# Optimization experiments

Hardware: AMD Instinct MI355X
Metric: run time of the kernel (lower is better)

The kernel has to match this reference:

```python
import jax, jax.numpy as jnp
import numpy as np

NUM_CLASSES = 80
STRIDES = (8, 16, 32)


def _decode(p, stride):
    # p: [B, 5+C, H, W] raw head -> [B, HW, 5+C] decoded (xy in px, wh=exp*stride)
    B, C, H, W = p.shape
    ys, xs = jnp.meshgrid(jnp.arange(H), jnp.arange(W), indexing='ij')
    grid = jnp.stack([xs, ys], -1).reshape(H * W, 2).astype(p.dtype)
    out = p.reshape(B, C, H * W).transpose(0, 2, 1)
    xy = (out[..., :2] + grid) * stride
    wh = jnp.exp(out[..., 2:4]) * stride
    out = jnp.concatenate([xy, wh, out[..., 4:]], -1)
    es = jnp.full((H * W,), float(stride), p.dtype)
    return out, grid[:, 0], grid[:, 1], es


def _pairwise_iou(gt, pr):
    # gt [G,4] cxcywh, pr [A,4] -> [G,A]
    gt_tl = gt[:, None, :2] - gt[:, None, 2:] * 0.5
    gt_br = gt[:, None, :2] + gt[:, None, 2:] * 0.5
    pr_tl = pr[None, :, :2] - pr[None, :, 2:] * 0.5
    pr_br = pr[None, :, :2] + pr[None, :, 2:] * 0.5
    tl = jnp.maximum(gt_tl, pr_tl)
    br = jnp.minimum(gt_br, pr_br)
    en = jnp.all(tl < br, -1).astype(gt.dtype)
    inter = jnp.prod(br - tl, -1) * en
    a_gt = jnp.prod(gt[:, 2:], -1)[:, None]
    a_pr = jnp.prod(pr[:, 2:], -1)[None, :]
    return inter / (a_gt + a_pr - inter + 1e-16)


def _assign(gt_boxes, gt_cls, bbox, clsp, objp, xg, yg, es):
    # SimOTA assignment for one image (all fixed-shape; non-candidate anchors
    # are masked out via huge cost instead of boolean gather).
    G = gt_boxes.shape[0]
    xc = (xg + 0.5) * es  # [A] anchor centers
    yc = (yg + 0.5) * es
    gl = gt_boxes[:, 0:1] - 0.5 * gt_boxes[:, 2:3]
    gr = gt_boxes[:, 0:1] + 0.5 * gt_boxes[:, 2:3]
    gt_ = gt_boxes[:, 1:2] - 0.5 * gt_boxes[:, 3:4]
    gb = gt_boxes[:, 1:2] + 0.5 * gt_boxes[:, 3:4]
    in_box = (xc[None] > gl) & (xc[None] < gr) & (yc[None] > gt_) & (yc[None] < gb)  # [G,A]
    r = 2.5 * es[None]
    in_ctr = ((xc[None] > gt_boxes[:, 0:1] - r) & (xc[None] < gt_boxes[:, 0:1] + r)
              & (yc[None] > gt_boxes[:, 1:2] - r) & (yc[None] < gt_boxes[:, 1:2] + r))
    fg_cand = jnp.any(in_box, 0) | jnp.any(in_ctr, 0)  # [A]
    in_both = in_box & in_ctr  # [G,A]

    ious = _pairwise_iou(gt_boxes, bbox)  # [G,A]
    ious_m = jnp.where(fg_cand[None, :], ious, 0.0)
    iou_cost = -jnp.log(ious_m + 1e-8)

    # pairwise cls BCE cost: bce(sqrt(sigmoid(cls)*sigmoid(obj)), onehot(gt)).sum(-1)
    p = jnp.sqrt(jax.nn.sigmoid(clsp) * jax.nn.sigmoid(objp[:, None]))  # [A,C]
    lp = jnp.maximum(jnp.log(p), -100.0)
    l1p = jnp.maximum(jnp.log1p(-p), -100.0)
    t = jax.nn.one_hot(gt_cls, NUM_CLASSES, dtype=p.dtype)  # [G,C]
    cls_cost = -(jnp.einsum('ac,gc->ga', lp - l1p, t) + jnp.sum(l1p, -1)[None, :])

    cost = (cls_cost + 3.0 * iou_cost
            + 1e5 * (~in_both).astype(p.dtype)
            + 1e9 * (~fg_cand)[None, :].astype(p.dtype))

    # dynamic-k: k_g = clamp(sum(top10 ious), min=1)
    topk_ious, _ = jax.lax.top_k(ious_m, 10)
    dyn_k = jnp.clip(topk_ious.sum(-1).astype(jnp.int32), 1, None)  # [G]
    rank = jnp.argsort(jnp.argsort(cost, axis=1), axis=1)  # rank of each anchor per gt
    matching = (rank < dyn_k[:, None]) & fg_cand[None, :]  # [G,A]
    # resolve anchors matched to multiple gts: keep min-cost gt
    multi = matching.sum(0) > 1
    best = jnp.argmin(cost, 0)
    matching = jnp.where(multi[None, :], jnp.arange(G)[:, None] == best[None, :], matching)

    fg = jnp.any(matching, 0)  # [A]
    matched_gt = jnp.argmax(matching, 0)  # [A]
    pred_iou = jnp.sum(matching * ious, 0)  # [A]
    matched_cls = gt_cls[matched_gt]
    return fg, matched_gt, pred_iou, matched_cls


def _giou_loss(b, g):
    tl = jnp.maximum(b[..., :2] - b[..., 2:] * 0.5, g[..., :2] - g[..., 2:] * 0.5)
    br = jnp.minimum(b[..., :2] + b[..., 2:] * 0.5, g[..., :2] + g[..., 2:] * 0.5)
    area_b = jnp.prod(b[..., 2:], -1)
    area_g = jnp.prod(g[..., 2:], -1)
    en = jnp.all(tl < br, -1).astype(b.dtype)
    inter = jnp.prod(br - tl, -1) * en
    union = area_b + area_g - inter
    iou = inter / (union + 1e-16)
    ctl = jnp.minimum(b[..., :2] - b[..., 2:] * 0.5, g[..., :2] - g[..., 2:] * 0.5)
    cbr = jnp.maximum(b[..., :2] + b[..., 2:] * 0.5, g[..., :2] + g[..., 2:] * 0.5)
    area_c = jnp.maximum(jnp.prod(cbr - ctl, -1), 1e-16)
    giou = iou - (area_c - union) / area_c
    return 1.0 - jnp.clip(giou, -1.0, 1.0)


def _bce_logits(x, t):
    return jnp.maximum(x, 0.0) - x * t + jnp.log1p(jnp.exp(-jnp.abs(x)))


def _forward(p8, p16, p32, labels):
    outs, xo, yo, eo = [], [], [], []
    for p, s in zip((p8, p16, p32), STRIDES):
        o, x, y, e = _decode(p, s)
        outs.append(o); xo.append(x); yo.append(y); eo.append(e)
    outputs = jnp.concatenate(outs, 1)  # [B, A, 5+C]
    xg = jnp.concatenate(xo); yg = jnp.concatenate(yo); es = jnp.concatenate(eo)

    bbox = outputs[..., :4]
    obj = outputs[..., 4]
    cls = outputs[..., 5:]
    gt_boxes = labels[..., :4]
    gt_cls = labels[..., 4].astype(jnp.int32)

    # assignment runs under no_grad in torch
    det = jax.lax.stop_gradient(outputs)
    fg, matched_gt, pred_iou, matched_cls = jax.vmap(
        lambda gb, gc, o: _assign(gb, gc, o[..., :4], o[..., 5:], o[..., 4], xg, yg, es)
    )(gt_boxes, gt_cls, det)

    fgf = fg.astype(outputs.dtype)  # [B,A]
    reg_t = jnp.take_along_axis(gt_boxes, matched_gt[..., None], axis=1)  # [B,A,4]
    cls_t = (jax.nn.one_hot(matched_cls, NUM_CLASSES, dtype=outputs.dtype)
             * pred_iou[..., None] * fgf[..., None])

    loss_iou = jnp.sum(_giou_loss(bbox, reg_t) * fgf)
    loss_obj = jnp.sum(_bce_logits(obj, fgf))
    loss_cls = jnp.sum(_bce_logits(cls, cls_t) * fgf[..., None])
    num_fg = jnp.maximum(jnp.sum(fgf), 1.0)
    return (5.0 * loss_iou + loss_obj + loss_cls) / num_fg


def setup_inputs() -> dict:
    key = jax.random.key(0)
    k1, k2, k3, k4, k5, k6 = jax.random.split(key, 6)
    B, NGT = 32, 20
    p8 = jax.random.normal(k1, (B, 5 + NUM_CLASSES, 80, 80), dtype=jnp.float32)
    p16 = jax.random.normal(k2, (B, 5 + NUM_CLASSES, 40, 40), dtype=jnp.float32)
    p32 = jax.random.normal(k3, (B, 5 + NUM_CLASSES, 20, 20), dtype=jnp.float32)
    cxy = jax.random.uniform(k4, (B, NGT, 2), dtype=jnp.float32, minval=32.0, maxval=608.0)
    wh = jax.random.uniform(k5, (B, NGT, 2), dtype=jnp.float32, minval=16.0, maxval=128.0)
    cls = jax.random.randint(k6, (B, NGT, 1), 0, NUM_CLASSES).astype(jnp.float32)
    labels = jnp.concatenate([cxy, wh, cls], -1)
    return {"p8": p8, "p16": p16, "p32": p32, "labels": labels}


def reference(p8, p16, p32, labels):
    return _forward(p8, p16, p32, labels)
```

## Files before the change

kernel.cpp:

```cpp
#include <hip/hip_runtime.h>
#include <cstdint>
#include <cstddef>

#define NA 8400
#define NAP 8448
#define NB 32
#define NG 20
#define NCL 80
#define NBLK 33

__device__ __forceinline__ float frcp(float x) { return __builtin_amdgcn_rcpf(x); }
__device__ __forceinline__ float bce0(float x) {
  return fmaxf(x, 0.0f) + __logf(1.0f + __expf(-fabsf(x)));
}

__device__ __forceinline__ void anchor_info(int a, const float* p8, const float* p16,
                                            const float* p32, int b, const float*& base,
                                            int& hw, int& HW, int& xg, int& yg, float& fs) {
  if (a < 6400)      { hw = a;        HW = 6400; xg = hw % 80; yg = hw / 80; fs = 8.f;
                       base = p8  + (size_t)b * 85 * 6400; }
  else if (a < 8000) { hw = a - 6400; HW = 1600; xg = hw % 40; yg = hw / 40; fs = 16.f;
                       base = p16 + (size_t)b * 85 * 1600; }
  else               { hw = a - 8000; HW = 400;  xg = hw % 20; yg = hw / 20; fs = 32.f;
                       base = p32 + (size_t)b * 85 * 400; }
}

__device__ __forceinline__ float iou_raw(float gx, float gy, float gw, float gh, float4 p) {
  float gtlx = gx - gw * 0.5f, gtly = gy - gh * 0.5f;
  float gbrx = gx + gw * 0.5f, gbry = gy + gh * 0.5f;
  float ptlx = p.x - p.z * 0.5f, ptly = p.y - p.w * 0.5f;
  float pbrx = p.x + p.z * 0.5f, pbry = p.y + p.w * 0.5f;
  float tlx = fmaxf(gtlx, ptlx), tly = fmaxf(gtly, ptly);
  float brx = fminf(gbrx, pbrx), bry = fminf(gbry, pbry);
  float inter = ((tlx < brx) && (tly < bry)) ? (brx - tlx) * (bry - tly) : 0.0f;
  float ag = gw * gh, ap = p.z * p.w;
  return inter * frcp(ag + ap - inter + 1e-16f);
}

__device__ __forceinline__ float cost_from_x(float x, float lso, float slr,
                                             unsigned int am, int g,
                                             float gx, float gy, float gw, float gh,
                                             float4 pb, float& iou_out) {
  float u = __logf(1.0f + __expf(-fabsf(x)));
  float lsx = fminf(x, 0.0f) - u;
  float lpr = 0.5f * (lsx + lso);
  float p   = __expf(lpr);
  float l1p = fmaxf(__logf(1.0f - p), -100.0f);
  float wv  = fmaxf(lpr, -100.0f) - l1p;
  float iou = iou_raw(gx, gy, gw, gh, pb);
  iou_out = iou;
  float cst = -(wv + slr) - 3.0f * __logf(iou + 1e-8f);
  if (!((am >> g) & 1u)) cst += 100000.0f;
  return cst;
}

__device__ __forceinline__ float giou_loss(float4 bb, float gx, float gy, float gw, float gh) {
  float btlx = bb.x - bb.z * 0.5f, btly = bb.y - bb.w * 0.5f;
  float bbrx = bb.x + bb.z * 0.5f, bbry = bb.y + bb.w * 0.5f;
  float gtlx = gx - gw * 0.5f, gtly = gy - gh * 0.5f;
  float gbrx = gx + gw * 0.5f, gbry = gy + gh * 0.5f;
  float tlx = fmaxf(btlx, gtlx), tly = fmaxf(btly, gtly);
  float brx = fminf(bbrx, gbrx), bry = fminf(bbry, gbry);
  float area_b = bb.z * bb.w, area_g = gw * gh;
  float inter = ((tlx < brx) && (tly < bry)) ? (brx - tlx) * (bry - tly) : 0.0f;
  float uni = area_b + area_g - inter;
  float iou = inter / (uni + 1e-16f);
  float ctlx = fminf(btlx, gtlx), ctly = fminf(btly, gtly);
  float cbrx = fmaxf(bbrx, gbrx), cbry = fmaxf(bbry, gbry);
  float area_c = fmaxf((cbrx - ctlx) * (cbry - ctly), 1e-16f);
  float giou = iou - (area_c - uni) / area_c;
  giou = fminf(fmaxf(giou, -1.0f), 1.0f);
  return 1.0f - giou;
}

__global__ __launch_bounds__(256) void kA(const float* __restrict__ p8,
                                          const float* __restrict__ p16,
                                          const float* __restrict__ p32,
                                          const float* __restrict__ labels,
                                          int* __restrict__ n_fg_cnt,
                                          float4* __restrict__ meta_c,
                                          float4* __restrict__ bbox_c,
                                          float* __restrict__ sb_c,
                                          float* __restrict__ x_tbl,
                                          unsigned int* __restrict__ match_c,
                                          float* __restrict__ blk_obj) {
  __shared__ float s_gt[NG * 4];
  __shared__ unsigned int s_c2g[NCL];
  __shared__ unsigned int s_wcnt[4];
  __shared__ float s_part[4];
  __shared__ unsigned int s_base;

  int blk = blockIdx.x, b = blockIdx.y, tid = threadIdx.x, lane = tid & 63, wid = tid >> 6;
  size_t bo = (size_t)b * NAP;

  if (tid < NCL) s_c2g[tid] = 0u;
  __syncthreads();
  if (tid < NG) {
    s_gt[tid * 4 + 0] = labels[((size_t)b * NG + tid) * 5 + 0];
    s_gt[tid * 4 + 1] = labels[((size_t)b * NG + tid) * 5 + 1];
    s_gt[tid * 4 + 2] = labels[((size_t)b * NG + tid) * 5 + 2];
    s_gt[tid * 4 + 3] = labels[((size_t)b * NG + tid) * 5 + 3];
    int c = (int)labels[((size_t)b * NG + tid) * 5 + 4];
    atomicOr(&s_c2g[c], 1u << tid);
  }
  __syncthreads();

  int a = blk * 256 + tid;
  match_c[bo + a] = 0u;
  bool fg = false;
  unsigned int msk = 0u;
  float bce_obj = 0.0f, obj = 0.0f;
  const float* base = nullptr; int hw = 0, HW = 0, xg = 0, yg = 0; float fs = 8.f;
  if (a < NA) {
    anchor_info(a, p8, p16, p32, b, base, hw, HW, xg, yg, fs);
    obj = base[4 * HW + hw];
    bce_obj = bce0(obj);
    float xc = ((float)xg + 0.5f) * fs;
    float yc = ((float)yg + 0.5f) * fs;
    float r = 2.5f * fs;
#pragma unroll
    for (int g = 0; g < NG; ++g) {
      float gx = s_gt[g * 4 + 0], gy = s_gt[g * 4 + 1];
      float gw = s_gt[g * 4 + 2], gh = s_gt[g * 4 + 3];
      bool inb = (xc > gx - 0.5f * gw) && (xc < gx + 0.5f * gw) &&
                 (yc > gy - 0.5f * gh) && (yc < gy + 0.5f * gh);
      bool inc = (xc > gx - r) && (xc < gx + r) && (yc > gy - r) && (yc < gy + r);
      fg = fg || inb || inc;
      if (inb && inc) msk |= (1u << g);
    }
  }

  unsigned long long bm = __ballot(fg);
#pragma unroll
  for (int off = 32; off; off >>= 1) bce_obj += __shfl_down(bce_obj, off, 64);
  if (lane == 0) { s_wcnt[wid] = (unsigned int)__popcll(bm); s_part[wid] = bce_obj; }
  __syncthreads();
  if (tid == 0) {
    unsigned int cnt = s_wcnt[0] + s_wcnt[1] + s_wcnt[2] + s_wcnt[3];
    s_base = cnt ? (unsigned int)atomicAdd(&n_fg_cnt[b], (int)cnt) : 0u;
    blk_obj[b * NBLK + blk] = s_part[0] + s_part[1] + s_part[2] + s_part[3];
  }
  __syncthreads();

  int ci = -1;
  if (fg) {
    unsigned int li = 0;
    for (int w = 0; w < wid; ++w) li += s_wcnt[w];
    li += (unsigned int)__popcll(bm & ((1ull << lane) - 1ull));
    ci = (int)(s_base + li);
  }

  float lso = 0.0f;
  if (a < NA) {
    float uo = __logf(1.0f + __expf(-fabsf(obj)));
    lso = fminf(obj, 0.0f) - uo;
  }

  float sb = 0.0f, sl = 0.0f;
  if (a < NA) {
    const float* cb = base + (size_t)5 * HW + hw;
#pragma unroll 8
    for (int c = 0; c < NCL; ++c) {
      float x = cb[(size_t)c * HW];
      float u = __logf(1.0f + __expf(-fabsf(x)));
      sb += fmaxf(x, 0.0f) + u;
      float lsx = fminf(x, 0.0f) - u;
      float lpr = 0.5f * (lsx + lso);
      float p   = __expf(lpr);
      sl += fmaxf(__logf(1.0f - p), -100.0f);
      unsigned int m = s_c2g[c];
      if (fg && m) {
        do {
          int g = __ffs(m) - 1; m &= m - 1u;
          x_tbl[((size_t)b * NG + g) * NAP + ci] = x;
        } while (m);
      }
    }
  }

  if (!fg) return;

  float v0 = base[hw];
  float v1 = base[HW + hw];
  float v2 = base[2 * HW + hw];
  float v3 = base[3 * HW + hw];
  float4 bb4 = make_float4((v0 + (float)xg) * fs, (v1 + (float)yg) * fs,
                           __expf(v2) * fs, __expf(v3) * fs);
  bbox_c[bo + ci] = bb4;
  sb_c[bo + ci] = sb;
  meta_c[bo + ci] = make_float4(lso, sl, __uint_as_float(msk), obj);
}

__global__ __launch_bounds__(256) void kBG(const float* __restrict__ labels,
                                           const int* __restrict__ n_fg,
                                           const float4* __restrict__ meta_c,
                                           const float4* __restrict__ bbox_c,
                                           const float* __restrict__ sb_c,
                                           const float* __restrict__ x_tbl,
                                           unsigned int* __restrict__ match_c,
                                           const float* __restrict__ blk_obj,
                                           float* __restrict__ accum,
                                           int* __restrict__ done_g,
                                           int* __restrict__ done_img,
                                           float* __restrict__ out) {
  __shared__ float s_gt[NG * 5];
  __shared__ float s_wt[4 * 10];
  __shared__ float s_wc[4 * 10];
  __shared__ int   s_wi[4 * 10];
  __shared__ float s_red[16];
  __shared__ int   s_flag;

  int g = blockIdx.x, b = blockIdx.y, tid = threadIdx.x;
  int lane = tid & 63, wid = tid >> 6;
  int n = n_fg[b];
  size_t bo = (size_t)b * NAP;
  const float* __restrict__ xrow = x_tbl + ((size_t)b * NG + g) * NAP;

  if (tid < NG * 5) s_gt[tid] = labels[(size_t)b * NG * 5 + tid];
  __syncthreads();

  float ggx = s_gt[g * 5], ggy = s_gt[g * 5 + 1];
  float ggw = s_gt[g * 5 + 2], ggh = s_gt[g * 5 + 3];

  float t10[10];
  float c10v[10];
  int   c10i[10];
#pragma unroll
  for (int j = 0; j < 10; ++j) { t10[j] = 0.0f; c10v[j] = 3.4e38f; c10i[j] = 0x7fffffff; }

  for (int ci = tid; ci < n; ci += 256) {
    float4 me = meta_c[bo + ci];
    float4 pb = bbox_c[bo + ci];
    float x = xrow[ci];
    unsigned int am = __float_as_uint(me.z);
    float iou;
    float cst = cost_from_x(x, me.x, me.y, am, g, ggx, ggy, ggw, ggh, pb, iou);
    if (iou > t10[9]) {
      t10[9] = iou;
#pragma unroll
      for (int q = 9; q > 0; --q) {
        if (t10[q] > t10[q - 1]) { float t = t10[q]; t10[q] = t10[q - 1]; t10[q - 1] = t; }
        else break;
      }
    }
    if (cst < c10v[9] || (cst == c10v[9] && ci < c10i[9])) {
      c10v[9] = cst; c10i[9] = ci;
#pragma unroll
      for (int q = 9; q > 0; --q) {
        if (c10v[q] < c10v[q - 1] ||
            (c10v[q] == c10v[q - 1] && c10i[q] < c10i[q - 1])) {
          float tv = c10v[q]; c10v[q] = c10v[q - 1]; c10v[q - 1] = tv;
          int   ti = c10i[q]; c10i[q] = c10i[q - 1]; c10i[q - 1] = ti;
        } else break;
      }
    }
  }

  for (int r = 0; r < 10; ++r) {
    float v = t10[0];
    float bv = v;
    float cv = c10v[0]; int cix = c10i[0];
    float cbv = cv;     int cbi = cix;
#pragma unroll
    for (int off = 32; off; off >>= 1) {
      bv = fmaxf(bv, __shfl_down(bv, off, 64));
      float ov = __shfl_down(cbv, off, 64);
      int   oi = __shfl_down(cbi, off, 64);
      if (ov < cbv || (ov == cbv && oi < cbi)) { cbv = ov; cbi = oi; }
    }
    bv  = __shfl(bv, 0, 64);
    cbv = __shfl(cbv, 0, 64);
    cbi = __shfl(cbi, 0, 64);
    unsigned long long won = __ballot(v == bv);
    if (lane == __ffsll(won) - 1) {
#pragma unroll
      for (int q = 0; q < 9; ++q) t10[q] = t10[q + 1];
      t10[9] = -1.0f;
    }
    if (cv == cbv && cix == cbi) {
#pragma unroll
      for (int q = 0; q < 9; ++q) { c10v[q] = c10v[q + 1]; c10i[q] = c10i[q + 1]; }
      c10v[9] = 3.4e38f; c10i[9] = 0x7fffffff;
    }
    if (lane == 0) {
      s_wt[wid * 10 + r] = bv;
      s_wc[wid * 10 + r] = cbv;
      s_wi[wid * 10 + r] = cbi;
    }
  }
  __syncthreads();

  if (tid == 0) {
    int p0 = 0, p1 = 0, p2 = 0, p3 = 0;
    float s = 0.0f;
    for (int r = 0; r < 10; ++r) {
      float v0 = (p0 < 10) ? s_wt[p0]      : -2.0f;
      float v1 = (p1 < 10) ? s_wt[10 + p1] : -2.0f;
      float v2 = (p2 < 10) ? s_wt[20 + p2] : -2.0f;
      float v3 = (p3 < 10) ? s_wt[30 + p3] : -2.0f;
      float m = fmaxf(fmaxf(v0, v1), fmaxf(v2, v3));
      s += m;
      if (m == v0) ++p0; else if (m == v1) ++p1; else if (m == v2) ++p2; else ++p3;
    }
    int k = (int)s;
    if (k < 1) k = 1;
    int q[4] = {0, 0, 0, 0};
    for (int it = 0; it < k; ++it) {
      float bv = 3.3e38f; int bi = 0x7fffffff; int sel = -1;
#pragma unroll
      for (int w = 0; w < 4; ++w) {
        if (q[w] < 10) {
          float v = s_wc[w * 10 + q[w]];
          int   i = s_wi[w * 10 + q[w]];
          if (v < bv || (v == bv && i < bi)) { bv = v; bi = i; sel = w; }
        }
      }
      if (sel < 0 || bv >= 1e37f) break;
      atomicOr(&match_c[bo + bi], 1u << g);
      ++q[sel];
    }
    __threadfence();
    s_flag = (atomicAdd(&done_g[b], 1) == NG - 1) ? 1 : 0;
  }
  __syncthreads();
  if (!s_flag) return;

  float li = 0.0f, oe = 0.0f, lc = 0.0f, nf = 0.0f;
  for (int ci = tid; ci < n; ci += 256) {
    unsigned int m = atomicOr(&match_c[bo + ci], 0u);
    if (m == 0u) continue;
    float4 me = meta_c[bo + ci];
    float4 pb = bbox_c[bo + ci];
    unsigned int am = __float_as_uint(me.z);
    int mg;
    if (m & (m - 1)) {
      float bestc = 3.4e38f; mg = 0;
      for (int gq = 0; gq < NG; ++gq) {
        float xq = x_tbl[((size_t)b * NG + gq) * NAP + ci];
        float iouq;
        float cq = cost_from_x(xq, me.x, me.y, am, gq, s_gt[gq * 5], s_gt[gq * 5 + 1],
                               s_gt[gq * 5 + 2], s_gt[gq * 5 + 3], pb, iouq);
        if (cq < bestc) { bestc = cq; mg = gq; }
      }
    } else {
      mg = __ffs(m) - 1;
    }
    float gx = s_gt[mg * 5], gy = s_gt[mg * 5 + 1];
    float gw = s_gt[mg * 5 + 2], gh = s_gt[mg * 5 + 3];
    float piou = iou_raw(gx, gy, gw, gh, pb);
    li += giou_loss(pb, gx, gy, gw, gh);
    float xcls = x_tbl[((size_t)b * NG + mg) * NAP + ci];
    lc += sb_c[bo + ci] - xcls * piou;
    oe += me.w;
    nf += 1.0f;
  }

  float vals[4] = {li, oe, lc, nf};
#pragma unroll
  for (int q2 = 0; q2 < 4; ++q2) {
#pragma unroll
    for (int off = 32; off; off >>= 1) vals[q2] += __shfl_down(vals[q2], off, 64);
  }
  if (lane == 0) {
    s_red[wid * 4 + 0] = vals[0];
    s_red[wid * 4 + 1] = vals[1];
    s_red[wid * 4 + 2] = vals[2];
    s_red[wid * 4 + 3] = vals[3];
  }
  __syncthreads();
  if (tid < 4) {
    const int slot[4] = {0, 2, 3, 4};
    float s = s_red[tid] + s_red[4 + tid] + s_red[8 + tid] + s_red[12 + tid];
    atomicAdd(&accum[slot[tid]], s);
  }

  if (tid == 0) {
    __threadfence();
    s_flag = (atomicAdd(done_img, 1) == NB - 1) ? 1 : 0;
  }
  __syncthreads();
  if (!s_flag) return;

  float s = 0.0f;
  for (int i = tid; i < NB * NBLK; i += 256) s += blk_obj[i];
#pragma unroll
  for (int off = 32; off; off >>= 1) s += __shfl_down(s, off, 64);
  if ((tid & 63) == 0) s_red[tid >> 6] = s;
  __syncthreads();
  if (tid == 0) {
    float obj_base = s_red[0] + s_red[1] + s_red[2] + s_red[3];
    float loss_iou = atomicAdd(&accum[0], 0.0f);
    float oex      = atomicAdd(&accum[2], 0.0f);
    float loss_cls = atomicAdd(&accum[3], 0.0f);
    float num_fg   = atomicAdd(&accum[4], 0.0f);
    float loss_obj = obj_base - oex;
    out[0] = (5.0f * loss_iou + loss_obj + loss_cls) / fmaxf(num_fg, 1.0f);
  }
}

extern "C" void kernel_launch(void* const* d_in, const int* in_sizes, int n_in,
                              void* d_out, int out_size, void* d_ws, size_t ws_size,
                              hipStream_t stream) {
  const float* p8     = (const float*)d_in[0];
  const float* p16    = (const float*)d_in[1];
  const float* p32    = (const float*)d_in[2];
  const float* labels = (const float*)d_in[3];
  float* out = (float*)d_out;

  const size_t BAP = (size_t)NB * NAP;
  char* w = (char*)d_ws;
  float4*       bbox_c   = (float4*)w;
  float4*       meta_c   = (float4*)(w + BAP * 16);
  float*        x_tbl    = (float*)(w + BAP * 32);
  char*         w2       = (char*)x_tbl + (size_t)NB * NG * NAP * 4;
  float*        sb_c     = (float*)(w2);
  unsigned int* match_c  = (unsigned int*)(w2 + BAP * 4);
  char*         w3       = w2 + BAP * 8;
  int*          n_fg     = (int*)w3;
  float*        accum    = (float*)(w3 + 128);
  int*          done_g   = (int*)(w3 + 256);
  int*          done_img = (int*)(w3 + 384);
  float*        blk_obj  = (float*)(w3 + 512);

  hipMemsetAsync(w3, 0, 512, stream);

  kA <<<dim3(NBLK, NB), dim3(256), 0, stream>>>(p8, p16, p32, labels, n_fg, meta_c,
                                                bbox_c, sb_c, x_tbl, match_c, blk_obj);
  kBG<<<dim3(NG, NB), dim3(256), 0, stream>>>(labels, n_fg, meta_c, bbox_c, sb_c, x_tbl,
                                              match_c, blk_obj, accum, done_g,
                                              done_img, out);
}
```

Baseline: 200.0 us.

## Split class-loop across warps with float4 vectorized loads and LDS reduction

Instead of each thread looping over all 80 class logits for its own anchor, each of the four warps now handles 20 classes for four consecutive anchors per lane, using float4 loads. Partial BCE sums are reduced through shared memory, and each thread's candidate index and obj log-sigmoid are shared through LDS. This shortens the per-thread dependent loop and widens memory transactions. In exchange it adds shared memory, extra barriers, and alignment assumptions on the float4 loads (HW values are multiples of 4, so the loads stay aligned).

```diff
diff --git a/kernel.cpp b/kernel.cpp
--- a/kernel.cpp
+++ b/kernel.cpp
@@ -86,6 +86,10 @@
                                           float* __restrict__ blk_obj) {
   __shared__ float s_gt[NG * 4];
   __shared__ unsigned int s_c2g[NCL];
+  __shared__ float s_lso[256];
+  __shared__ int   s_ci[256];
+  __shared__ float s_sb[4][256];
+  __shared__ float s_sl[4][256];
   __shared__ unsigned int s_wcnt[4];
   __shared__ float s_part[4];
   __shared__ unsigned int s_base;
@@ -142,53 +146,81 @@
   }
   __syncthreads();
 
+  float lso = 0.0f;
+  if (a < NA) {
+    float uo = __logf(1.0f + __expf(-fabsf(obj)));
+    lso = fminf(obj, 0.0f) - uo;
+  }
+  s_lso[tid] = lso;
+
   int ci = -1;
   if (fg) {
     unsigned int li = 0;
     for (int w = 0; w < wid; ++w) li += s_wcnt[w];
     li += (unsigned int)__popcll(bm & ((1ull << lane) - 1ull));
     ci = (int)(s_base + li);
-  }
-
-  float lso = 0.0f;
-  if (a < NA) {
-    float uo = __logf(1.0f + __expf(-fabsf(obj)));
-    lso = fminf(obj, 0.0f) - uo;
-  }
-
-  float sb = 0.0f, sl = 0.0f;
-  if (a < NA) {
-    const float* cb = base + (size_t)5 * HW + hw;
-#pragma unroll 8
-    for (int c = 0; c < NCL; ++c) {
-      float x = cb[(size_t)c * HW];
-      float u = __logf(1.0f + __expf(-fabsf(x)));
-      sb += fmaxf(x, 0.0f) + u;
-      float lsx = fminf(x, 0.0f) - u;
-      float lpr = 0.5f * (lsx + lso);
-      float p   = __expf(lpr);
-      sl += fmaxf(__logf(1.0f - p), -100.0f);
+    float v0 = base[hw];
+    float v1 = base[HW + hw];
+    float v2 = base[2 * HW + hw];
+    float v3 = base[3 * HW + hw];
+    bbox_c[bo + ci] = make_float4((v0 + (float)xg) * fs, (v1 + (float)yg) * fs,
+                                  __expf(v2) * fs, __expf(v3) * fs);
+  }
+  s_ci[tid] = ci;
+  __syncthreads();
+
+  int a0 = blk * 256 + (lane << 2);
+  bool valid = a0 < NA;
+  const float* vbase = nullptr; int vhw = 0, vHW = 0, dxg, dyg; float dfs;
+  if (valid) anchor_info(a0, p8, p16, p32, b, vbase, vhw, vHW, dxg, dyg, dfs);
+  float l4[4], sb4[4] = {0.f, 0.f, 0.f, 0.f}, sl4[4] = {0.f, 0.f, 0.f, 0.f};
+  int   ci4[4];
+#pragma unroll
+  for (int j = 0; j < 4; ++j) {
+    l4[j]  = s_lso[(lane << 2) + j];
+    ci4[j] = s_ci[(lane << 2) + j];
+  }
+
+  if (valid) {
+    const float* cb = vbase + (size_t)5 * vHW + vhw;
+#pragma unroll 4
+    for (int cc = 0; cc < 20; ++cc) {
+      int c = wid * 20 + cc;
+      float4 x4 = *reinterpret_cast<const float4*>(cb + (size_t)c * vHW);
+      float xa[4] = {x4.x, x4.y, x4.z, x4.w};
+#pragma unroll
+      for (int j = 0; j < 4; ++j) {
+        float x = xa[j];
+        float u = __logf(1.0f + __expf(-fabsf(x)));
+        sb4[j] += fmaxf(x, 0.0f) + u;
+        float lsx = fminf(x, 0.0f) - u;
+        float lpr = 0.5f * (lsx + l4[j]);
+        float p   = __expf(lpr);
+        sl4[j] += fmaxf(__logf(1.0f - p), -100.0f);
+      }
       unsigned int m = s_c2g[c];
-      if (fg && m) {
-        do {
-          int g = __ffs(m) - 1; m &= m - 1u;
-          x_tbl[((size_t)b * NG + g) * NAP + ci] = x;
-        } while (m);
-      }
-    }
-  }
-
-  if (!fg) return;
-
-  float v0 = base[hw];
-  float v1 = base[HW + hw];
-  float v2 = base[2 * HW + hw];
-  float v3 = base[3 * HW + hw];
-  float4 bb4 = make_float4((v0 + (float)xg) * fs, (v1 + (float)yg) * fs,
-                           __expf(v2) * fs, __expf(v3) * fs);
-  bbox_c[bo + ci] = bb4;
-  sb_c[bo + ci] = sb;
-  meta_c[bo + ci] = make_float4(lso, sl, __uint_as_float(msk), obj);
+      while (m) {
+        int g = __ffs(m) - 1; m &= m - 1u;
+        size_t rowo = ((size_t)b * NG + g) * NAP;
+#pragma unroll
+        for (int j = 0; j < 4; ++j)
+          if (ci4[j] >= 0) x_tbl[rowo + ci4[j]] = xa[j];
+      }
+    }
+  }
+#pragma unroll
+  for (int j = 0; j < 4; ++j) {
+    s_sb[wid][(lane << 2) + j] = sb4[j];
+    s_sl[wid][(lane << 2) + j] = sl4[j];
+  }
+  __syncthreads();
+
+  if (ci >= 0) {
+    float sb = ((s_sb[0][tid] + s_sb[1][tid]) + s_sb[2][tid]) + s_sb[3][tid];
+    float sl = ((s_sl[0][tid] + s_sl[1][tid]) + s_sl[2][tid]) + s_sl[3][tid];
+    sb_c[bo + ci] = sb;
+    meta_c[bo + ci] = make_float4(lso, sl, __uint_as_float(msk), obj);
+  }
 }
 
 __global__ __launch_bounds__(256) void kBG(const float* __restrict__ labels,
```

New measurement: 194.6 us. 2.7% less time.
